# Optimization experiments

Hardware: AMD Instinct MI355X
Metric: run time of the kernel (lower is better)

Reference implementation:

```python
import jax, jax.numpy as jnp
import numpy as np

B, L, IN, H, NC = 256, 200, 512, 256, 1


def _gru_layer(x, w_ih, w_hh, b_ih, b_hh, reverse):
    # x: [B, L, F]; w_ih: [3H, F]; w_hh: [3H, H]
    xi = jnp.einsum('blf,gf->blg', x, w_ih) + b_ih  # precompute input gates [B,L,3H]

    def step(h, xi_t):
        gh = h @ w_hh.T + b_hh
        i_r, i_z, i_n = jnp.split(xi_t, 3, axis=-1)
        h_r, h_z, h_n = jnp.split(gh, 3, axis=-1)
        r = jax.nn.sigmoid(i_r + h_r)
        z = jax.nn.sigmoid(i_z + h_z)
        n = jnp.tanh(i_n + r * h_n)
        h_new = (1.0 - z) * n + z * h
        return h_new, h_new

    h0 = jnp.zeros((x.shape[0], H), dtype=x.dtype)
    _, out = jax.lax.scan(step, h0, jnp.swapaxes(xi, 0, 1), reverse=reverse)
    return jnp.swapaxes(out, 0, 1)  # [B, L, H], time-aligned with input


def setup_inputs() -> dict:
    key = jax.random.key(0)
    ks = iter(jax.random.split(key, 32))
    d = {"x": jax.random.normal(next(ks), (B, L, IN), dtype=jnp.float32)}
    s = 0.05
    for layer, fin in ((0, IN), (1, 2 * H)):
        for suf in ('', 'r'):
            d[f'w_ih_l{layer}{suf}'] = jax.random.normal(next(ks), (3 * H, fin)) * s
            d[f'w_hh_l{layer}{suf}'] = jax.random.normal(next(ks), (3 * H, H)) * s
            d[f'b_ih_l{layer}{suf}'] = jax.random.normal(next(ks), (3 * H,)) * s
            d[f'b_hh_l{layer}{suf}'] = jax.random.normal(next(ks), (3 * H,)) * s
    d['fc1_w'] = jax.random.normal(next(ks), (NC, 2 * H)) * s
    d['fc1_b'] = jax.random.normal(next(ks), (NC,)) * s
    d['fc2_w'] = jax.random.normal(next(ks), (NC * 10, 2 * H)) * s
    d['fc2_b'] = jax.random.normal(next(ks), (NC * 10,)) * s
    return d


def reference(x, w_ih_l0, w_hh_l0, b_ih_l0, b_hh_l0,
              w_ih_l0r, w_hh_l0r, b_ih_l0r, b_hh_l0r,
              w_ih_l1, w_hh_l1, b_ih_l1, b_hh_l1,
              w_ih_l1r, w_hh_l1r, b_ih_l1r, b_hh_l1r,
              fc1_w, fc1_b, fc2_w, fc2_b):
    bs = x.shape[0]
    # dropout is identity in eval mode
    l0 = jnp.concatenate([
        _gru_layer(x, w_ih_l0, w_hh_l0, b_ih_l0, b_hh_l0, False),
        _gru_layer(x, w_ih_l0r, w_hh_l0r, b_ih_l0r, b_hh_l0r, True),
    ], axis=-1)
    out = jnp.concatenate([
        _gru_layer(l0, w_ih_l1, w_hh_l1, b_ih_l1, b_hh_l1, False),
        _gru_layer(l0, w_ih_l1r, w_hh_l1r, b_ih_l1r, b_hh_l1r, True),
    ], axis=-1)  # [B, L, 2H]
    y = (out @ fc1_w.T + fc1_b).squeeze(-1)            # [B, L]
    y2 = (out @ fc2_w.T + fc2_b).reshape(bs, -1)        # [B, L*10]
    p = jax.nn.softmax(y, axis=1)[:, :, None] / 10.0    # [B, L, 1]
    y3 = jnp.broadcast_to(p, (bs, y.shape[1], 10)).reshape(bs, -1) + jax.nn.softmax(y2, axis=1)
    return (y, y2, y3)
```

## Files before the change

kernel.cpp:

```cpp
#include <hip/hip_runtime.h>


typedef _Float16 half8 __attribute__((ext_vector_type(8)));
typedef _Float16 half4v __attribute__((ext_vector_type(4)));
typedef float fx4 __attribute__((ext_vector_type(4)));

#define BATCH 256
#define SEQ   200
#define HID   256
#define MROWS (BATCH*SEQ)
#define NG    1536
#define KDIM  512

__device__ __forceinline__ void gload_lds16(const _Float16* g, _Float16* l) {
  __builtin_amdgcn_global_load_lds((const __attribute__((address_space(1))) void*)g,
                                   (__attribute__((address_space(3))) void*)l, 16, 0, 0);
}

__device__ __forceinline__ void gru_barrier() {
  asm volatile("s_waitcnt lgkmcnt(0)\n\ts_barrier" ::: "memory");
}

__device__ __forceinline__ float lo16f(unsigned v) {
  return (float)__builtin_bit_cast(_Float16, (unsigned short)(v & 0xffffu));
}
__device__ __forceinline__ float hi16f(unsigned v) {
  return (float)__builtin_bit_cast(_Float16, (unsigned short)(v >> 16));
}


__global__ __launch_bounds__(256) void k_cast_x(const float4* __restrict__ x,
                                                half4v* __restrict__ xh, int n4) {
  int i = blockIdx.x * 256 + threadIdx.x;
  if (i < n4) {
    float4 v = x[i];
    half4v o;
    o[0] = (_Float16)v.x; o[1] = (_Float16)v.y; o[2] = (_Float16)v.z; o[3] = (_Float16)v.w;
    xh[i] = o;
  }
}

__global__ __launch_bounds__(256) void k_prep_wih(const float* __restrict__ wf,
                                                  const float* __restrict__ wr,
                                                  const float* __restrict__ bf_,
                                                  const float* __restrict__ br_,
                                                  const float* __restrict__ bhf,
                                                  const float* __restrict__ bhr,
                                                  _Float16* __restrict__ wcat,
                                                  float* __restrict__ bcat) {
  int idx = blockIdx.x * 256 + threadIdx.x;
  int n = idx >> 9;
  float v = (n < 768) ? wf[idx] : wr[idx - 768 * 512];
  wcat[idx] = (_Float16)v;
  if (idx < 1536) {
    float b;
    if (idx < 768) b = bf_[idx] + ((idx < 512) ? bhf[idx] : 0.f);
    else { int i2 = idx - 768; b = br_[i2] + ((i2 < 512) ? bhr[i2] : 0.f); }
    bcat[idx] = b;
  }
}

__global__ __launch_bounds__(256) void k_prep_whh(const float* __restrict__ whf,
                                                  const float* __restrict__ whr,
                                                  _Float16* __restrict__ whp) {
  int e = blockIdx.x * 256 + threadIdx.x;
  int dir = e / 196608;
  int r = e - dir * 196608;
  int w = r / 12288;  int r2 = r - w * 12288;
  int gate = r2 >> 12; int r3 = r2 & 4095;
  int kf = r3 >> 9;    int r4 = r3 & 511;
  int lane = r4 >> 3;  int i = r4 & 7;
  int row = gate * 256 + w * 16 + (lane & 15);
  int col = kf * 32 + (lane >> 4) * 8 + i;
  const float* src = dir ? whr : whf;
  whp[e] = (_Float16)src[row * 256 + col];
}

__global__ __launch_bounds__(256) void k_gemm(const _Float16* __restrict__ A,
                                              const _Float16* __restrict__ Wt,
                                              const float* __restrict__ bias,
                                              _Float16* __restrict__ C) {
  __shared__ __align__(16) _Float16 As[128 * 32];
  __shared__ __align__(16) _Float16 Bs[128 * 32];
  const int tid = threadIdx.x;
  const int wv = tid >> 6, ln = tid & 63;
  const int wm = wv >> 1, wn = wv & 1;
  const int jl = ln & 15, q = ln >> 4;

  const int lid  = blockIdx.x + 400 * blockIdx.y;
  const int xcd  = lid & 7;
  const int slot = lid >> 3;
  const int mi   = xcd * 50 + (slot / 12);
  const int ni   = slot % 12;
  const int m0 = mi * 128, n0 = ni * 128;

  const int r0 = tid >> 2, k80 = (tid & 3) * 8;
  const int r1 = r0 + 64;

  fx4 acc[4][4];
#pragma unroll
  for (int a = 0; a < 4; ++a)
#pragma unroll
    for (int b = 0; b < 4; ++b) acc[a][b] = (fx4){0.f, 0.f, 0.f, 0.f};

  for (int kk = 0; kk < KDIM; kk += 32) {
    gload_lds16(A  + (size_t)(m0 + r0) * KDIM + kk + k80, As + tid * 8);
    gload_lds16(A  + (size_t)(m0 + r1) * KDIM + kk + k80, As + (tid + 256) * 8);
    gload_lds16(Wt + (size_t)(n0 + r0) * KDIM + kk + k80, Bs + tid * 8);
    gload_lds16(Wt + (size_t)(n0 + r1) * KDIM + kk + k80, Bs + (tid + 256) * 8);
    __syncthreads();
    half8 af[4], bfr[4];
#pragma unroll
    for (int mt = 0; mt < 4; ++mt)
      af[mt] = *(const half8*)(As + (wm * 64 + mt * 16 + jl) * 32 + q * 8);
#pragma unroll
    for (int nt = 0; nt < 4; ++nt)
      bfr[nt] = *(const half8*)(Bs + (wn * 64 + nt * 16 + jl) * 32 + q * 8);
#pragma unroll
    for (int mt = 0; mt < 4; ++mt)
#pragma unroll
      for (int nt = 0; nt < 4; ++nt)
        acc[mt][nt] = __builtin_amdgcn_mfma_f32_16x16x32_f16(af[mt], bfr[nt], acc[mt][nt], 0, 0, 0);
    __syncthreads();
  }

  float bsv[4];
#pragma unroll
  for (int nt = 0; nt < 4; ++nt) bsv[nt] = bias[n0 + wn * 64 + nt * 16 + jl];

#pragma unroll
  for (int mt = 0; mt < 4; ++mt) {
#pragma unroll
    for (int ntp = 0; ntp < 2; ++ntp) {
#pragma unroll
      for (int rg = 0; rg < 4; ++rg) {
        const int grow = m0 + wm * 64 + mt * 16 + q * 4 + rg;
        _Float16 lo = (_Float16)(acc[mt][2 * ntp][rg]     + bsv[2 * ntp]);
        _Float16 hi = (_Float16)(acc[mt][2 * ntp + 1][rg] + bsv[2 * ntp + 1]);
        unsigned pk = (unsigned)__builtin_bit_cast(unsigned short, lo)
                    | ((unsigned)__builtin_bit_cast(unsigned short, hi) << 16);
        *(unsigned*)(C + (size_t)grow * NG + n0 + wn * 64 + ntp * 32 + jl * 2) = pk;
      }
    }
  }
}

__global__ __launch_bounds__(512) __attribute__((amdgpu_waves_per_eu(2, 2)))
void k_gru(const _Float16* __restrict__ xi,
           const _Float16* __restrict__ whp,
           const float* __restrict__ bhhf,
           const float* __restrict__ bhhr,
           _Float16* __restrict__ out) {
  extern __shared__ _Float16 smem[];
  _Float16* nlds = smem;
  _Float16* hb0  = smem + 65536;
  _Float16* hb1  = smem + 69632;

  const int tid = threadIdx.x, w = tid >> 6, ln = tid & 63;
  const int jl = ln & 15, q = ln >> 4;
  const int bt = blockIdx.x, dir = blockIdx.y;
  const float* bhh = dir ? bhhr : bhhf;

  half8 wrz[2][2][8];
#pragma unroll
  for (int tt = 0; tt < 2; ++tt) {
    const _Float16* wb = whp + ((size_t)(dir * 16 + w * 2 + tt)) * 12288;
#pragma unroll
    for (int g = 0; g < 2; ++g)
#pragma unroll
      for (int kf = 0; kf < 8; ++kf) {
        wrz[tt][g][kf] = *(const half8*)(wb + g * 4096 + kf * 512 + ln * 8);
        asm volatile("" : "+v"(wrz[tt][g][kf]));
      }
#pragma unroll
    for (int kf = 0; kf < 8; ++kf)
      *(half8*)(nlds + ((w * 2 + tt) * 8 + kf) * 512 + ln * 8) =
          *(const half8*)(wb + 2 * 4096 + kf * 512 + ln * 8);
  }
  float bhn[2];
#pragma unroll
  for (int tt = 0; tt < 2; ++tt) bhn[tt] = bhh[512 + w * 32 + tt * 16 + jl];

  for (int i = tid; i < 4096; i += 512) hb0[i] = (_Float16)0.f;

  const long long t0 = dir ? (SEQ - 1) : 0;
  const int xstep = dir ? -NG : NG;
  const int wcol2 = w * 32 + jl * 2;
  const _Float16* xp[4];
#pragma unroll
  for (int rg = 0; rg < 4; ++rg)
    xp[rg] = xi + ((size_t)((bt * 16 + q * 4 + rg) * SEQ) + t0) * NG + dir * 768;

  unsigned cx[3][4];
#pragma unroll
  for (int rg = 0; rg < 4; ++rg)
#pragma unroll
    for (int g = 0; g < 3; ++g)
      cx[g][rg] = *(const unsigned*)(xp[rg] + g * 256 + wcol2);

  const int orow = tid >> 5, oc = tid & 31;
  _Float16* op = out + ((size_t)((bt * 16 + orow) * SEQ) + t0) * 512 + dir * 256 + oc * 8;
  const int ostep = dir ? -512 : 512;
  const int oaddr = orow * 256 + ((oc ^ (orow & 7)) << 3);

  float hprev[2][4] = {{0.f,0.f,0.f,0.f},{0.f,0.f,0.f,0.f}};
  __syncthreads();

  for (int t = 0; t < SEQ; ++t) {
    const _Float16* hr = (t & 1) ? hb1 : hb0;
    _Float16*       hw = (t & 1) ? hb0 : hb1;

    unsigned nx[3][4];
    if (t < SEQ - 1) {
#pragma unroll
      for (int rg = 0; rg < 4; ++rg) {
        const _Float16* p = xp[rg] + xstep;
#pragma unroll
        for (int g = 0; g < 3; ++g)
          nx[g][rg] = *(const unsigned*)(p + g * 256 + wcol2);
      }
    }

    fx4 acc[2][3];
#pragma unroll
    for (int rg = 0; rg < 4; ++rg) {
      const unsigned c0 = cx[0][rg], c1 = cx[1][rg];
      acc[0][0][rg] = lo16f(c0);
      acc[1][0][rg] = hi16f(c0);
      acc[0][1][rg] = lo16f(c1);
      acc[1][1][rg] = hi16f(c1);
      acc[0][2][rg] = bhn[0];
      acc[1][2][rg] = bhn[1];
    }

    if (t > 0) {
      *(half8*)op = *(const half8*)(hr + oaddr);
      op += ostep;
    }

#pragma unroll
    for (int kf = 0; kf < 8; ++kf) {
      int cc = kf * 4 + q;
      half8 a = *(const half8*)(hr + jl * 256 + ((cc ^ (jl & 7)) << 3));
      half8 nb0 = *(const half8*)(nlds + ((w * 2 + 0) * 8 + kf) * 512 + ln * 8);
      half8 nb1 = *(const half8*)(nlds + ((w * 2 + 1) * 8 + kf) * 512 + ln * 8);
      acc[0][0] = __builtin_amdgcn_mfma_f32_16x16x32_f16(a, wrz[0][0][kf], acc[0][0], 0, 0, 0);
      acc[0][1] = __builtin_amdgcn_mfma_f32_16x16x32_f16(a, wrz[0][1][kf], acc[0][1], 0, 0, 0);
      acc[0][2] = __builtin_amdgcn_mfma_f32_16x16x32_f16(a, nb0,           acc[0][2], 0, 0, 0);
      acc[1][0] = __builtin_amdgcn_mfma_f32_16x16x32_f16(a, wrz[1][0][kf], acc[1][0], 0, 0, 0);
      acc[1][1] = __builtin_amdgcn_mfma_f32_16x16x32_f16(a, wrz[1][1][kf], acc[1][1], 0, 0, 0);
      acc[1][2] = __builtin_amdgcn_mfma_f32_16x16x32_f16(a, nb1,           acc[1][2], 0, 0, 0);
    }

#pragma unroll
    for (int tt = 0; tt < 2; ++tt) {
      const int col = w * 32 + jl + tt * 16;
      const int chunk = col >> 3;
#pragma unroll
      for (int rg = 0; rg < 4; ++rg) {
        const int rr = q * 4 + rg;
        const int haddr = rr * 256 + ((chunk ^ (rr & 7)) << 3) + (jl & 7);
        float xn = tt ? hi16f(cx[2][rg]) : lo16f(cx[2][rg]);
        float rv = __builtin_amdgcn_rcpf(1.f + __expf(-acc[tt][0][rg]));
        float zv = __builtin_amdgcn_rcpf(1.f + __expf(-acc[tt][1][rg]));
        float gn = fmaf(rv, acc[tt][2][rg], xn);
        float e2 = __expf(2.f * gn);
        float nn = fmaf(-2.f, __builtin_amdgcn_rcpf(e2 + 1.f), 1.f);
        float hp = hprev[tt][rg];
        float h = fmaf(zv, hp - nn, nn);
        hprev[tt][rg] = h;
        hw[haddr] = (_Float16)h;
      }
    }
#pragma unroll
    for (int rg = 0; rg < 4; ++rg) {
      xp[rg] += (t < SEQ - 1) ? xstep : 0;
#pragma unroll
      for (int g = 0; g < 3; ++g) cx[g][rg] = nx[g][rg];
    }
    gru_barrier();
  }
  *(half8*)op = *(const half8*)(hb0 + oaddr);
}


__global__ __launch_bounds__(256) void k_heads1(const _Float16* __restrict__ out,
                                                const float* __restrict__ fc1w,
                                                const float* __restrict__ fc1b,
                                                const float* __restrict__ fc2w,
                                                const float* __restrict__ fc2b,
                                                float* __restrict__ y,
                                                float* __restrict__ y2) {
  const int tid = threadIdx.x, wv = tid >> 6, ln = tid & 63;

  float4 w1a = *(const float4*)(fc1w + ln * 8);
  float4 w1b = *(const float4*)(fc1w + ln * 8 + 4);
  float4 wa[10], wb[10];
#pragma unroll
  for (int c = 0; c < 10; ++c) {
    wa[c] = *(const float4*)(fc2w + c * 512 + ln * 8);
    wb[c] = *(const float4*)(fc2w + c * 512 + ln * 8 + 4);
  }
  float b1 = fc1b[0];
  float b2[10];
#pragma unroll
  for (int c = 0; c < 10; ++c) b2[c] = fc2b[c];

#pragma unroll
  for (int i = 0; i < 4; ++i) {
    int gw = blockIdx.x * 16 + wv * 4 + i;
    int b = gw / SEQ, t = gw - b * SEQ;
    half8 ov = *(const half8*)(out + (size_t)gw * 512 + ln * 8);
    float o[8];
#pragma unroll
    for (int k = 0; k < 8; ++k) o[k] = (float)ov[k];

    float s1 = o[0]*w1a.x + o[1]*w1a.y + o[2]*w1a.z + o[3]*w1a.w
             + o[4]*w1b.x + o[5]*w1b.y + o[6]*w1b.z + o[7]*w1b.w;
    float s2[10];
#pragma unroll
    for (int c = 0; c < 10; ++c) {
      s2[c] = o[0]*wa[c].x + o[1]*wa[c].y + o[2]*wa[c].z + o[3]*wa[c].w
            + o[4]*wb[c].x + o[5]*wb[c].y + o[6]*wb[c].z + o[7]*wb[c].w;
    }
#pragma unroll
    for (int m = 32; m; m >>= 1) {
      s1 += __shfl_xor(s1, m);
#pragma unroll
      for (int c = 0; c < 10; ++c) s2[c] += __shfl_xor(s2[c], m);
    }
    if (ln == 0) {
      y[gw] = s1 + b1;
      float* y2p = y2 + (size_t)b * 2000 + t * 10;
#pragma unroll
      for (int c = 0; c < 10; ++c) y2p[c] = s2[c] + b2[c];
    }
  }
}

__device__ __forceinline__ float blkRedMax(float v, float* red, int tid) {
#pragma unroll
  for (int m = 32; m; m >>= 1) v = fmaxf(v, __shfl_xor(v, m));
  __syncthreads();
  if ((tid & 63) == 0) red[tid >> 6] = v;
  __syncthreads();
  return fmaxf(fmaxf(red[0], red[1]), fmaxf(red[2], red[3]));
}
__device__ __forceinline__ float blkRedSum(float v, float* red, int tid) {
#pragma unroll
  for (int m = 32; m; m >>= 1) v += __shfl_xor(v, m);
  __syncthreads();
  if ((tid & 63) == 0) red[tid >> 6] = v;
  __syncthreads();
  return red[0] + red[1] + red[2] + red[3];
}

__global__ __launch_bounds__(256) void k_heads2(const float* __restrict__ y,
                                                const float* __restrict__ y2,
                                                float* __restrict__ y3) {
  __shared__ float sp[SEQ];
  __shared__ float se[2000];
  __shared__ float red[4];
  int b = blockIdx.x, tid = threadIdx.x;

  float v = (tid < SEQ) ? y[(size_t)b * SEQ + tid] : -3.0e38f;
  float mx = blkRedMax(v, red, tid);
  float e = (tid < SEQ) ? __expf(v - mx) : 0.f;
  float sum = blkRedSum(e, red, tid);
  if (tid < SEQ) sp[tid] = e / (sum * 10.f);

  float vv[8];
  float lm = -3.0e38f;
#pragma unroll
  for (int r = 0; r < 8; ++r) {
    int k = tid + r * 256;
    vv[r] = (k < 2000) ? y2[(size_t)b * 2000 + k] : -3.0e38f;
    lm = fmaxf(lm, vv[r]);
  }
  float mx2 = blkRedMax(lm, red, tid);
  float ls = 0.f;
#pragma unroll
  for (int r = 0; r < 8; ++r) {
    int k = tid + r * 256;
    if (k < 2000) { float ee = __expf(vv[r] - mx2); se[k] = ee; ls += ee; }
  }
  float sum2 = blkRedSum(ls, red, tid);
  __syncthreads();
  float inv = 1.f / sum2;
#pragma unroll
  for (int r = 0; r < 8; ++r) {
    int k = tid + r * 256;
    if (k < 2000) y3[(size_t)b * 2000 + k] = se[k] * inv + sp[k / 10];
  }
}


extern "C" void kernel_launch(void* const* d_in, const int* in_sizes, int n_in,
                              void* d_out, int out_size, void* d_ws, size_t ws_size,
                              hipStream_t stream) {
  const float* x     = (const float*)d_in[0];
  const float* wih0  = (const float*)d_in[1];
  const float* whh0  = (const float*)d_in[2];
  const float* bih0  = (const float*)d_in[3];
  const float* bhh0  = (const float*)d_in[4];
  const float* wih0r = (const float*)d_in[5];
  const float* whh0r = (const float*)d_in[6];
  const float* bih0r = (const float*)d_in[7];
  const float* bhh0r = (const float*)d_in[8];
  const float* wih1  = (const float*)d_in[9];
  const float* whh1  = (const float*)d_in[10];
  const float* bih1  = (const float*)d_in[11];
  const float* bhh1  = (const float*)d_in[12];
  const float* wih1r = (const float*)d_in[13];
  const float* whh1r = (const float*)d_in[14];
  const float* bih1r = (const float*)d_in[15];
  const float* bhh1r = (const float*)d_in[16];
  const float* fc1w  = (const float*)d_in[17];
  const float* fc1b  = (const float*)d_in[18];
  const float* fc2w  = (const float*)d_in[19];
  const float* fc2b  = (const float*)d_in[20];

  char* ws = (char*)d_ws;
  _Float16* xh    = (_Float16*)(ws + 0);
  _Float16* xi    = (_Float16*)(ws + 52428800);
  _Float16* l0    = (_Float16*)(ws + 209715200);
  _Float16* outh  = (_Float16*)(ws + 262144000);
  _Float16* wcat0 = (_Float16*)(ws + 314572800);
  _Float16* wcat1 = (_Float16*)(ws + 316145664);
  _Float16* whp0  = (_Float16*)(ws + 317718528);
  _Float16* whp1  = (_Float16*)(ws + 318504960);
  float*    bcat0 = (float*)(ws + 319291392);
  float*    bcat1 = (float*)(ws + 319297536);

  float* y  = (float*)d_out;
  float* y2 = (float*)d_out + 51200;
  float* y3 = (float*)d_out + 563200;

  k_cast_x<<<25600, 256, 0, stream>>>((const float4*)x, (half4v*)xh, 6553600);
  k_prep_wih<<<3072, 256, 0, stream>>>(wih0, wih0r, bih0, bih0r, bhh0, bhh0r, wcat0, bcat0);
  k_prep_wih<<<3072, 256, 0, stream>>>(wih1, wih1r, bih1, bih1r, bhh1, bhh1r, wcat1, bcat1);
  k_prep_whh<<<1536, 256, 0, stream>>>(whh0, whh0r, whp0);
  k_prep_whh<<<1536, 256, 0, stream>>>(whh1, whh1r, whp1);

  hipFuncSetAttribute(reinterpret_cast<const void*>(k_gru),
                      hipFuncAttributeMaxDynamicSharedMemorySize, 147456);

  k_gemm<<<dim3(400, 12), 256, 0, stream>>>(xh, wcat0, bcat0, xi);
  k_gru<<<dim3(16, 2), 512, 147456, stream>>>(xi, whp0, bhh0, bhh0r, l0);
  k_gemm<<<dim3(400, 12), 256, 0, stream>>>(l0, wcat1, bcat1, xi);
  k_gru<<<dim3(16, 2), 512, 147456, stream>>>(xi, whp1, bhh1, bhh1r, outh);
  k_heads1<<<3200, 256, 0, stream>>>(outh, fc1w, fc1b, fc2w, fc2b, y, y2);
  k_heads2<<<256, 256, 0, stream>>>(y, y2, y3);
}
```

Before: 1.156 ms.

## Widen GEMM K-tile to 64 with XOR-swizzled LDS and merge prep kernels

The input-projection GEMM now stages a 64-wide K slice per iteration instead of 32, halving the number of barrier pairs. LDS rows are XOR-swizzled so that the 128-byte row stride does not cause bank conflicts on fragment reads. The four weight-prep kernels are merged into one launch to cut launch overhead. LDS use doubles to 32 KB per block, which may reduce occupancy.

```diff
diff --git a/kernel.cpp b/kernel.cpp
--- a/kernel.cpp
+++ b/kernel.cpp
@@ -40,15 +40,9 @@
   }
 }
 
-__global__ __launch_bounds__(256) void k_prep_wih(const float* __restrict__ wf,
-                                                  const float* __restrict__ wr,
-                                                  const float* __restrict__ bf_,
-                                                  const float* __restrict__ br_,
-                                                  const float* __restrict__ bhf,
-                                                  const float* __restrict__ bhr,
-                                                  _Float16* __restrict__ wcat,
-                                                  float* __restrict__ bcat) {
-  int idx = blockIdx.x * 256 + threadIdx.x;
+__device__ __forceinline__ void prep_wih_body(int idx,
+    const float* wf, const float* wr, const float* bf_, const float* br_,
+    const float* bhf, const float* bhr, _Float16* wcat, float* bcat) {
   int n = idx >> 9;
   float v = (n < 768) ? wf[idx] : wr[idx - 768 * 512];
   wcat[idx] = (_Float16)v;
@@ -60,10 +54,8 @@
   }
 }
 
-__global__ __launch_bounds__(256) void k_prep_whh(const float* __restrict__ whf,
-                                                  const float* __restrict__ whr,
-                                                  _Float16* __restrict__ whp) {
-  int e = blockIdx.x * 256 + threadIdx.x;
+__device__ __forceinline__ void prep_whh_body(int e,
+    const float* whf, const float* whr, _Float16* whp) {
   int dir = e / 196608;
   int r = e - dir * 196608;
   int w = r / 12288;  int r2 = r - w * 12288;
@@ -76,12 +68,37 @@
   whp[e] = (_Float16)src[row * 256 + col];
 }
 
+__global__ __launch_bounds__(256) void k_prep_all(
+    const float* __restrict__ wih0, const float* __restrict__ wih0r,
+    const float* __restrict__ bih0, const float* __restrict__ bih0r,
+    const float* __restrict__ bhh0, const float* __restrict__ bhh0r,
+    _Float16* __restrict__ wcat0, float* __restrict__ bcat0,
+    const float* __restrict__ wih1, const float* __restrict__ wih1r,
+    const float* __restrict__ bih1, const float* __restrict__ bih1r,
+    const float* __restrict__ bhh1, const float* __restrict__ bhh1r,
+    _Float16* __restrict__ wcat1, float* __restrict__ bcat1,
+    const float* __restrict__ whh0, const float* __restrict__ whh0r,
+    _Float16* __restrict__ whp0,
+    const float* __restrict__ whh1, const float* __restrict__ whh1r,
+    _Float16* __restrict__ whp1) {
+  const int b = blockIdx.x, tid = threadIdx.x;
+  if (b < 3072) {
+    prep_wih_body(b * 256 + tid, wih0, wih0r, bih0, bih0r, bhh0, bhh0r, wcat0, bcat0);
+  } else if (b < 6144) {
+    prep_wih_body((b - 3072) * 256 + tid, wih1, wih1r, bih1, bih1r, bhh1, bhh1r, wcat1, bcat1);
+  } else if (b < 7680) {
+    prep_whh_body((b - 6144) * 256 + tid, whh0, whh0r, whp0);
+  } else {
+    prep_whh_body((b - 7680) * 256 + tid, whh1, whh1r, whp1);
+  }
+}
+
 __global__ __launch_bounds__(256) void k_gemm(const _Float16* __restrict__ A,
                                               const _Float16* __restrict__ Wt,
                                               const float* __restrict__ bias,
                                               _Float16* __restrict__ C) {
-  __shared__ __align__(16) _Float16 As[128 * 32];
-  __shared__ __align__(16) _Float16 Bs[128 * 32];
+  __shared__ __align__(16) _Float16 As[128 * 64];
+  __shared__ __align__(16) _Float16 Bs[128 * 64];
   const int tid = threadIdx.x;
   const int wv = tid >> 6, ln = tid & 63;
   const int wm = wv >> 1, wn = wv & 1;
@@ -94,33 +111,44 @@
   const int ni   = slot % 12;
   const int m0 = mi * 128, n0 = ni * 128;
 
-  const int r0 = tid >> 2, k80 = (tid & 3) * 8;
-  const int r1 = r0 + 64;
-
   fx4 acc[4][4];
 #pragma unroll
   for (int a = 0; a < 4; ++a)
 #pragma unroll
     for (int b = 0; b < 4; ++b) acc[a][b] = (fx4){0.f, 0.f, 0.f, 0.f};
 
-  for (int kk = 0; kk < KDIM; kk += 32) {
-    gload_lds16(A  + (size_t)(m0 + r0) * KDIM + kk + k80, As + tid * 8);
-    gload_lds16(A  + (size_t)(m0 + r1) * KDIM + kk + k80, As + (tid + 256) * 8);
-    gload_lds16(Wt + (size_t)(n0 + r0) * KDIM + kk + k80, Bs + tid * 8);
-    gload_lds16(Wt + (size_t)(n0 + r1) * KDIM + kk + k80, Bs + (tid + 256) * 8);
+  for (int kk = 0; kk < KDIM; kk += 64) {
+#pragma unroll
+    for (int i = 0; i < 4; ++i) {
+      const int ch = tid + 256 * i;
+      const int r = ch >> 3, c = ch & 7;
+      const int sc = ((c ^ (r & 7)) << 3);
+      gload_lds16(A  + (size_t)(m0 + r) * KDIM + kk + sc, As + ch * 8);
+      gload_lds16(Wt + (size_t)(n0 + r) * KDIM + kk + sc, Bs + ch * 8);
+    }
     __syncthreads();
-    half8 af[4], bfr[4];
-#pragma unroll
-    for (int mt = 0; mt < 4; ++mt)
-      af[mt] = *(const half8*)(As + (wm * 64 + mt * 16 + jl) * 32 + q * 8);
-#pragma unroll
-    for (int nt = 0; nt < 4; ++nt)
-      bfr[nt] = *(const half8*)(Bs + (wn * 64 + nt * 16 + jl) * 32 + q * 8);
-#pragma unroll
-    for (int mt = 0; mt < 4; ++mt)
-#pragma unroll
-      for (int nt = 0; nt < 4; ++nt)
-        acc[mt][nt] = __builtin_amdgcn_mfma_f32_16x16x32_f16(af[mt], bfr[nt], acc[mt][nt], 0, 0, 0);
+    half8 af[2][4], bfr[2][4];
+#pragma unroll
+    for (int kh = 0; kh < 2; ++kh) {
+      const int wc = kh * 4 + q;
+#pragma unroll
+      for (int mt = 0; mt < 4; ++mt) {
+        const int row = wm * 64 + mt * 16 + jl;
+        af[kh][mt] = *(const half8*)(As + row * 64 + ((wc ^ (row & 7)) << 3));
+      }
+#pragma unroll
+      for (int nt = 0; nt < 4; ++nt) {
+        const int row = wn * 64 + nt * 16 + jl;
+        bfr[kh][nt] = *(const half8*)(Bs + row * 64 + ((wc ^ (row & 7)) << 3));
+      }
+    }
+#pragma unroll
+    for (int kh = 0; kh < 2; ++kh)
+#pragma unroll
+      for (int mt = 0; mt < 4; ++mt)
+#pragma unroll
+        for (int nt = 0; nt < 4; ++nt)
+          acc[mt][nt] = __builtin_amdgcn_mfma_f32_16x16x32_f16(af[kh][mt], bfr[kh][nt], acc[mt][nt], 0, 0, 0);
     __syncthreads();
   }
 
@@ -437,10 +465,9 @@
   float* y3 = (float*)d_out + 563200;
 
   k_cast_x<<<25600, 256, 0, stream>>>((const float4*)x, (half4v*)xh, 6553600);
-  k_prep_wih<<<3072, 256, 0, stream>>>(wih0, wih0r, bih0, bih0r, bhh0, bhh0r, wcat0, bcat0);
-  k_prep_wih<<<3072, 256, 0, stream>>>(wih1, wih1r, bih1, bih1r, bhh1, bhh1r, wcat1, bcat1);
-  k_prep_whh<<<1536, 256, 0, stream>>>(whh0, whh0r, whp0);
-  k_prep_whh<<<1536, 256, 0, stream>>>(whh1, whh1r, whp1);
+  k_prep_all<<<9216, 256, 0, stream>>>(wih0, wih0r, bih0, bih0r, bhh0, bhh0r, wcat0, bcat0,
+                                       wih1, wih1r, bih1, bih1r, bhh1, bhh1r, wcat1, bcat1,
+                                       whh0, whh0r, whp0, whh1, whh1r, whp1);
 
   hipFuncSetAttribute(reinterpret_cast<const void*>(k_gru),
                       hipFuncAttributeMaxDynamicSharedMemorySize, 147456);
```

After: 1.136 ms. No clear change (-1.8%).
